# Kernel tuning notes

Measured on AMD Instinct MI355X. Metric: run time of the kernel, lower is better.

## Reference

```python
import jax, jax.numpy as jnp
import numpy as np

BN_EPS = 1e-5

def _conv1x1(x, w, b):
    # x: [B,C,H,W], w: [O,C], b: [O] -> [B,O,H,W]
    return jnp.einsum('bchw,oc->bohw', x, w) + b[None, :, None, None]

def setup_inputs() -> dict:
    key = jax.random.key(0)
    ks = jax.random.split(key, 9)
    B, C, H, W = 8, 256, 64, 64
    I = C // 2
    s_in = 1.0 / np.sqrt(C)
    s_out = 1.0 / np.sqrt(I)
    return {
        'x':       jax.random.normal(ks[0], (B, C, H, W), dtype=jnp.float32),
        'g_w':     jax.random.uniform(ks[1], (I, C), jnp.float32, -s_in, s_in),
        'g_b':     jax.random.uniform(ks[2], (I,),  jnp.float32, -s_in, s_in),
        'theta_w': jax.random.uniform(ks[3], (I, C), jnp.float32, -s_in, s_in),
        'theta_b': jax.random.uniform(ks[4], (I,),  jnp.float32, -s_in, s_in),
        'phi_w':   jax.random.uniform(ks[5], (I, C), jnp.float32, -s_in, s_in),
        'phi_b':   jax.random.uniform(ks[6], (I,),  jnp.float32, -s_in, s_in),
        'w_w':     jax.random.uniform(ks[7], (C, I), jnp.float32, -s_out, s_out),
        'w_b':     jax.random.uniform(ks[8], (C,),  jnp.float32, -s_out, s_out),
        'gamma':   jnp.ones((C,), dtype=jnp.float32),   # BN weight init constant 1
        'beta':    jnp.zeros((C,), dtype=jnp.float32),  # BN bias init constant 0
    }

def reference(x, g_w, g_b, theta_w, theta_b, phi_w, phi_b, w_w, w_b, gamma, beta):
    B, C, H, W = x.shape
    I = g_w.shape[0]
    N = H * W
    g_x     = _conv1x1(x, g_w, g_b).reshape(B, I, N)          # [B,I,N]
    theta_x = _conv1x1(x, theta_w, theta_b).reshape(B, I, N)  # [B,I,N]
    phi_x   = _conv1x1(x, phi_w, phi_b).reshape(B, I, N)      # [B,I,N]
    # f = theta^T @ phi : [B,N,N]
    f = jnp.einsum('bin,bim->bnm', theta_x, phi_x)
    a = jax.nn.softmax(f, axis=-1)
    # y = a @ g^T : [B,N,I] -> [B,I,H,W]
    y = jnp.einsum('bnm,bim->bin', a, g_x).reshape(B, I, H, W)
    wy = _conv1x1(y, w_w, w_b)                                # [B,C,H,W]
    # BatchNorm2d (training mode: batch statistics over B,H,W per channel)
    mean = jnp.mean(wy, axis=(0, 2, 3), keepdims=True)
    var = jnp.var(wy, axis=(0, 2, 3), keepdims=True)
    wy_bn = (wy - mean) * jax.lax.rsqrt(var + BN_EPS)
    wy_bn = wy_bn * gamma[None, :, None, None] + beta[None, :, None, None]
    return wy_bn + x
```

## Files before the change

### kernel.cpp

```cpp
#include <hip/hip_runtime.h>

#define B_ 8
#define C_ 256
#define I_ 128
#define N_ 4096
#define BN_ (B_ * N_)
#define LOG2E 1.4426950408889634f

typedef __attribute__((ext_vector_type(8))) short bf16x8;
typedef __attribute__((ext_vector_type(4))) float f32x4;
typedef __attribute__((ext_vector_type(2))) int i32x2;

static __device__ __forceinline__ short f2bf(float f) {
    unsigned u = __float_as_uint(f);
    unsigned r = u + 0x7fffu + ((u >> 16) & 1u);
    return (short)(r >> 16);
}
static __device__ __forceinline__ float bf2f(short s) {
    return __uint_as_float(((unsigned)(unsigned short)s) << 16);
}
static __device__ __forceinline__ unsigned cvt_pk_bf16(float lo, float hi) {
    unsigned r;
    asm("v_cvt_pk_bf16_f32 %0, %1, %2" : "=v"(r) : "v"(lo), "v"(hi));
    return r;
}

__global__ void k_prep(const float* g_w, const float* theta_w, const float* phi_w,
                       const float* g_b, const float* theta_b, const float* phi_b,
                       const float* w_w, short* wcat, short* wwb, float* bcat) {
    int i = blockIdx.x * 256 + threadIdx.x;
    if (i < 384 * 256) {
        int j = i >> 8, c = i & 255;
        float v = (j < 128) ? theta_w[j * 256 + c] * LOG2E
                : (j < 256) ? phi_w[(j - 128) * 256 + c]
                            : g_w[(j - 256) * 256 + c];
        wcat[i] = f2bf(v);
    } else if (i < 384 * 256 + 256 * 128) {
        int k = i - 384 * 256;
        wwb[k] = f2bf(w_w[k]);
    } else if (i < 384 * 256 + 256 * 128 + 384) {
        int j = i - (384 * 256 + 256 * 128);
        bcat[j] = (j < 128) ? theta_b[j] * LOG2E
                : (j < 256) ? phi_b[j - 128] : g_b[j - 256];
    }
}

__global__ __launch_bounds__(256) void k_proj(const float* __restrict__ x,
                                              const short* __restrict__ wcat,
                                              const float* __restrict__ bcat,
                                              short* __restrict__ tp,
                                              short* __restrict__ gmat) {
    int b = blockIdx.y;
    int n0 = blockIdx.x * 64;
    int tid = threadIdx.x;
    int wave = tid >> 6, lane = tid & 63, s = lane & 15, q = lane >> 4;
    __shared__ short xs[64][264];

#pragma unroll
    for (int it = 0; it < 16; ++it) {
        int cr = (tid >> 4) + it * 16;
        int nc = tid & 15;
        const float4 v = *(const float4*)&x[((size_t)b * C_ + cr) * N_ + n0 + nc * 4];
        xs[nc * 4 + 0][cr] = f2bf(v.x);
        xs[nc * 4 + 1][cr] = f2bf(v.y);
        xs[nc * 4 + 2][cr] = f2bf(v.z);
        xs[nc * 4 + 3][cr] = f2bf(v.w);
    }
    __syncthreads();

    f32x4 acc[4][6];
#pragma unroll
    for (int rt = 0; rt < 4; ++rt)
#pragma unroll
        for (int jt = 0; jt < 6; ++jt) acc[rt][jt] = (f32x4){0.f, 0.f, 0.f, 0.f};

#pragma unroll
    for (int kb = 0; kb < 8; ++kb) {
        bf16x8 af[4], bfv[6];
#pragma unroll
        for (int rt = 0; rt < 4; ++rt)
            af[rt] = *(const bf16x8*)&xs[rt * 16 + s][kb * 32 + q * 8];
#pragma unroll
        for (int jt = 0; jt < 6; ++jt)
            bfv[jt] = *(const bf16x8*)&wcat[(wave * 96 + jt * 16 + s) * 256 + kb * 32 + q * 8];
#pragma unroll
        for (int rt = 0; rt < 4; ++rt)
#pragma unroll
            for (int jt = 0; jt < 6; ++jt)
                acc[rt][jt] = __builtin_amdgcn_mfma_f32_16x16x32_bf16(af[rt], bfv[jt], acc[rt][jt], 0, 0, 0);
    }

#pragma unroll
    for (int rt = 0; rt < 4; ++rt)
#pragma unroll
        for (int jt = 0; jt < 6; ++jt) {
            int j = wave * 96 + jt * 16 + s;
            float bias = bcat[j];
#pragma unroll
            for (int r = 0; r < 4; ++r) {
                int n = n0 + rt * 16 + 4 * q + r;
                float v = acc[rt][jt][r] + bias;
                if (j < 256)
                    tp[((size_t)b * N_ + n) * 256 + j] = f2bf(v);
                else
                    gmat[((size_t)b * I_ + (j - 256)) * N_ + n] = f2bf(v);
            }
        }
}

__global__ __launch_bounds__(256) void k_attn(const short* __restrict__ tp,
                                              const short* __restrict__ gmat,
                                              float* __restrict__ Op,
                                              float* __restrict__ lbuf) {
    int id = blockIdx.x;
    int b = id & 7;
    int qt = (id >> 3) & 31;
    int half = id >> 8;
    int n0 = qt * 128;
    int tid = threadIdx.x;
    int wave = tid >> 6, lane = tid & 63, s = lane & 15, q = lane >> 4;

    __shared__ __align__(16) short Kt[64 * 128];
    __shared__ __align__(16) short Vt[128 * 64];
    __shared__ __align__(16) short Pl[4 * 32 * 64];

    char* KtB = (char*)Kt;
    char* VtB = (char*)Vt;
    char* PlB = (char*)Pl;

    const int swz = (s & 7) << 4;
    int kA[4];
#pragma unroll
    for (int kb = 0; kb < 4; ++kb) kA[kb] = s * 256 + ((kb * 64 + q * 16) ^ swz);
    int vA[2];
    int pR[2];
#pragma unroll
    for (int kb2 = 0; kb2 < 2; ++kb2) {
        int col = (kb2 * 64 + q * 16) ^ swz;
        vA[kb2] = s * 128 + col;
        pR[kb2] = wave * 4096 + s * 128 + col;
    }
    int pW[4];
#pragma unroll
    for (int tc = 0; tc < 4; ++tc)
        pW[tc] = wave * 4096 + s * 128 + ((tc * 32 + q * 8) ^ swz);
    int krow = tid >> 4, kch = tid & 15;
    int vrow = tid >> 3, vch = tid & 7;
    int kW = krow * 256 + ((kch * 16) ^ ((krow & 7) << 4));
    int vW = vrow * 128 + ((vch * 16) ^ ((vrow & 7) << 4));

    bf16x8 qf[2][4];
#pragma unroll
    for (int fr = 0; fr < 2; ++fr) {
        const short* qb = tp + ((size_t)b * N_ + n0 + wave * 32 + fr * 16 + s) * 256;
#pragma unroll
        for (int kb = 0; kb < 4; ++kb) qf[fr][kb] = *(const bf16x8*)(qb + kb * 32 + q * 8);
    }

    f32x4 ot[2][8];
#pragma unroll
    for (int fr = 0; fr < 2; ++fr)
#pragma unroll
        for (int t = 0; t < 8; ++t) ot[fr][t] = (f32x4){0.f, 0.f, 0.f, 0.f};
    float lsum[2] = {0.f, 0.f};

    const int mStart = half * 2048, mEnd = mStart + 2048;

    bf16x8 pk[4], pv[4];
#pragma unroll
    for (int it = 0; it < 4; ++it) {
        pk[it] = *(const bf16x8*)&tp[((size_t)b * N_ + mStart + krow + it * 16) * 256 + 128 + kch * 8];
        pv[it] = *(const bf16x8*)&gmat[((size_t)b * I_ + vrow + it * 32) * N_ + mStart + vch * 8];
    }

    for (int m0 = mStart; m0 < mEnd; m0 += 64) {
        __syncthreads();
#pragma unroll
        for (int it = 0; it < 4; ++it) {
            *(bf16x8*)(KtB + kW + it * 4096) = pk[it];
            *(bf16x8*)(VtB + vW + it * 4096) = pv[it];
        }
        __syncthreads();
        if (m0 + 64 < mEnd) {
#pragma unroll
            for (int it = 0; it < 4; ++it) {
                pk[it] = *(const bf16x8*)&tp[((size_t)b * N_ + m0 + 64 + krow + it * 16) * 256 + 128 + kch * 8];
                pv[it] = *(const bf16x8*)&gmat[((size_t)b * I_ + vrow + it * 32) * N_ + m0 + 64 + vch * 8];
            }
        }

        f32x4 sa[2][4];
#pragma unroll
        for (int fr = 0; fr < 2; ++fr)
#pragma unroll
            for (int tc = 0; tc < 4; ++tc) sa[fr][tc] = (f32x4){0.f, 0.f, 0.f, 0.f};
#pragma unroll
        for (int tc = 0; tc < 4; ++tc) {
            bf16x8 bfv[4];
#pragma unroll
            for (int kb = 0; kb < 4; ++kb)
                bfv[kb] = *(const bf16x8*)(KtB + kA[kb] + tc * 4096);
#pragma unroll
            for (int fr = 0; fr < 2; ++fr)
#pragma unroll
                for (int kb = 0; kb < 4; ++kb)
                    sa[fr][tc] = __builtin_amdgcn_mfma_f32_16x16x32_bf16(bfv[kb], qf[fr][kb], sa[fr][tc], 0, 0, 0);
        }

#pragma unroll
        for (int fr = 0; fr < 2; ++fr) {
#pragma unroll
            for (int tc = 0; tc < 4; ++tc)
#pragma unroll
                for (int r = 0; r < 4; ++r) sa[fr][tc][r] = exp2f(sa[fr][tc][r]);
            float t0 = (sa[fr][0][0] + sa[fr][0][1]) + (sa[fr][0][2] + sa[fr][0][3]);
            float t1 = (sa[fr][1][0] + sa[fr][1][1]) + (sa[fr][1][2] + sa[fr][1][3]);
            float t2 = (sa[fr][2][0] + sa[fr][2][1]) + (sa[fr][2][2] + sa[fr][2][3]);
            float t3 = (sa[fr][3][0] + sa[fr][3][1]) + (sa[fr][3][2] + sa[fr][3][3]);
            lsum[fr] += (t0 + t1) + (t2 + t3);
#pragma unroll
            for (int tc = 0; tc < 4; ++tc) {
                i32x2 w;
                w.x = (int)cvt_pk_bf16(sa[fr][tc][0], sa[fr][tc][1]);
                w.y = (int)cvt_pk_bf16(sa[fr][tc][2], sa[fr][tc][3]);
                *(i32x2*)(PlB + pW[tc] + fr * 2048) = w;
            }
        }

#pragma unroll
        for (int kb2 = 0; kb2 < 2; ++kb2) {
            bf16x8 pa0 = *(const bf16x8*)(PlB + pR[kb2]);
            bf16x8 pa1 = *(const bf16x8*)(PlB + pR[kb2] + 2048);
#pragma unroll
            for (int t = 0; t < 8; ++t) {
                bf16x8 vb = *(const bf16x8*)(VtB + vA[kb2] + t * 2048);
                ot[0][t] = __builtin_amdgcn_mfma_f32_16x16x32_bf16(pa0, vb, ot[0][t], 0, 0, 0);
                ot[1][t] = __builtin_amdgcn_mfma_f32_16x16x32_bf16(pa1, vb, ot[1][t], 0, 0, 0);
            }
        }
    }

#pragma unroll
    for (int fr = 0; fr < 2; ++fr) {
        lsum[fr] += __shfl_xor(lsum[fr], 16);
        lsum[fr] += __shfl_xor(lsum[fr], 32);
    }
    if (q == 0) {
#pragma unroll
        for (int fr = 0; fr < 2; ++fr) {
            size_t row = (size_t)half * BN_ + (size_t)b * N_ + n0 + wave * 32 + fr * 16 + s;
            lbuf[row] = lsum[fr];
        }
    }

#pragma unroll
    for (int fr = 0; fr < 2; ++fr) {
        size_t rbase = (size_t)half * BN_ + (size_t)b * N_ + n0 + wave * 32 + fr * 16 + 4 * q;
#pragma unroll
        for (int t = 0; t < 8; ++t)
#pragma unroll
            for (int r = 0; r < 4; ++r)
                Op[(rbase + r) * I_ + t * 16 + s] = ot[fr][t][r];
    }
}

__global__ __launch_bounds__(256) void k_wy(const float* __restrict__ Op,
                                            const float* __restrict__ lbuf,
                                            const short* __restrict__ wwb,
                                            const float* __restrict__ w_b,
                                            short* __restrict__ wyh) {
    int b = blockIdx.y;
    int n0 = blockIdx.x * 64;
    int tid = threadIdx.x;
    int wave = tid >> 6, lane = tid & 63, s = lane & 15, q = lane >> 4;

    float linv[4];
#pragma unroll
    for (int nt = 0; nt < 4; ++nt) {
        size_t rn = (size_t)b * N_ + n0 + nt * 16 + s;
        linv[nt] = 1.0f / (lbuf[rn] + lbuf[(size_t)BN_ + rn]);
    }

    f32x4 acc[4][4];
#pragma unroll
    for (int ct = 0; ct < 4; ++ct)
#pragma unroll
        for (int nt = 0; nt < 4; ++nt) acc[ct][nt] = (f32x4){0.f, 0.f, 0.f, 0.f};
#pragma unroll
    for (int kb = 0; kb < 4; ++kb) {
        bf16x8 af[4], bfv[4];
#pragma unroll
        for (int ct = 0; ct < 4; ++ct)
            af[ct] = *(const bf16x8*)&wwb[(wave * 64 + ct * 16 + s) * 128 + kb * 32 + q * 8];
#pragma unroll
        for (int nt = 0; nt < 4; ++nt) {
            size_t rn = (size_t)b * N_ + n0 + nt * 16 + s;
            const float* p1 = Op + rn * I_ + kb * 32 + q * 8;
            const float* p2 = p1 + (size_t)BN_ * I_;
            float4 a0 = *(const float4*)p1;
            float4 a1 = *(const float4*)(p1 + 4);
            float4 b0 = *(const float4*)p2;
            float4 b1 = *(const float4*)(p2 + 4);
            short v[8];
            v[0] = f2bf((a0.x + b0.x) * linv[nt]);
            v[1] = f2bf((a0.y + b0.y) * linv[nt]);
            v[2] = f2bf((a0.z + b0.z) * linv[nt]);
            v[3] = f2bf((a0.w + b0.w) * linv[nt]);
            v[4] = f2bf((a1.x + b1.x) * linv[nt]);
            v[5] = f2bf((a1.y + b1.y) * linv[nt]);
            v[6] = f2bf((a1.z + b1.z) * linv[nt]);
            v[7] = f2bf((a1.w + b1.w) * linv[nt]);
            bfv[nt] = *(const bf16x8*)v;
        }
#pragma unroll
        for (int ct = 0; ct < 4; ++ct)
#pragma unroll
            for (int nt = 0; nt < 4; ++nt)
                acc[ct][nt] = __builtin_amdgcn_mfma_f32_16x16x32_bf16(af[ct], bfv[nt], acc[ct][nt], 0, 0, 0);
    }
#pragma unroll
    for (int ct = 0; ct < 4; ++ct)
#pragma unroll
        for (int nt = 0; nt < 4; ++nt)
#pragma unroll
            for (int r = 0; r < 4; ++r) {
                int c = wave * 64 + ct * 16 + 4 * q + r;
                int n = n0 + nt * 16 + s;
                wyh[((size_t)b * C_ + c) * N_ + n] = f2bf(acc[ct][nt][r] + w_b[c]);
            }
}

__global__ __launch_bounds__(256) void k_stats(const short* __restrict__ wyh,
                                               const float* __restrict__ gamma,
                                               const float* __restrict__ beta,
                                               float* __restrict__ scale,
                                               float* __restrict__ shift) {
    int c = blockIdx.x;
    int tid = threadIdx.x;
    float s1 = 0.f, s2 = 0.f;
    for (int b = 0; b < B_; ++b) {
        const short* p = wyh + ((size_t)b * C_ + c) * N_;
        for (int idx = tid * 8; idx < N_; idx += 2048) {
            bf16x8 v = *(const bf16x8*)&p[idx];
#pragma unroll
            for (int j = 0; j < 8; ++j) {
                float f = bf2f(v[j]);
                s1 += f;
                s2 += f * f;
            }
        }
    }
#pragma unroll
    for (int off = 1; off < 64; off <<= 1) {
        s1 += __shfl_xor(s1, off);
        s2 += __shfl_xor(s2, off);
    }
    __shared__ float r1[4], r2[4];
    if ((tid & 63) == 0) { r1[tid >> 6] = s1; r2[tid >> 6] = s2; }
    __syncthreads();
    if (tid == 0) {
        float t1 = r1[0] + r1[1] + r1[2] + r1[3];
        float t2 = r2[0] + r2[1] + r2[2] + r2[3];
        const float inv = 1.0f / 32768.0f;
        float mean = t1 * inv;
        float var = t2 * inv - mean * mean;
        float sc = gamma[c] * rsqrtf(var + 1e-5f);
        scale[c] = sc;
        shift[c] = beta[c] - mean * sc;
    }
}

__global__ __launch_bounds__(256) void k_out(const short* __restrict__ wyh,
                                             const float* __restrict__ x,
                                             const float* __restrict__ scale,
                                             const float* __restrict__ shift,
                                             float* __restrict__ out) {
    int gid = blockIdx.x * 256 + threadIdx.x;
    size_t base = (size_t)gid * 8;
    int c = (int)((base >> 12) & 255);
    float sc = scale[c], sh = shift[c];
    bf16x8 w = *(const bf16x8*)&wyh[base];
    float4 x0 = *(const float4*)&x[base];
    float4 x1 = *(const float4*)&x[base + 4];
    float4 o0, o1;
    o0.x = bf2f(w[0]) * sc + sh + x0.x;
    o0.y = bf2f(w[1]) * sc + sh + x0.y;
    o0.z = bf2f(w[2]) * sc + sh + x0.z;
    o0.w = bf2f(w[3]) * sc + sh + x0.w;
    o1.x = bf2f(w[4]) * sc + sh + x1.x;
    o1.y = bf2f(w[5]) * sc + sh + x1.y;
    o1.z = bf2f(w[6]) * sc + sh + x1.z;
    o1.w = bf2f(w[7]) * sc + sh + x1.w;
    *(float4*)&out[base] = o0;
    *(float4*)&out[base + 4] = o1;
}

extern "C" void kernel_launch(void* const* d_in, const int* in_sizes, int n_in,
                              void* d_out, int out_size, void* d_ws, size_t ws_size,
                              hipStream_t stream) {
    const float* x       = (const float*)d_in[0];
    const float* g_w     = (const float*)d_in[1];
    const float* g_b     = (const float*)d_in[2];
    const float* theta_w = (const float*)d_in[3];
    const float* theta_b = (const float*)d_in[4];
    const float* phi_w   = (const float*)d_in[5];
    const float* phi_b   = (const float*)d_in[6];
    const float* w_w     = (const float*)d_in[7];
    const float* w_b     = (const float*)d_in[8];
    const float* gamma   = (const float*)d_in[9];
    const float* beta    = (const float*)d_in[10];

    char* ws = (char*)d_ws;
    size_t off = 0;
    auto alloc = [&](size_t bytes) {
        void* p = ws + off;
        off += (bytes + 255) & ~(size_t)255;
        return p;
    };
    short*  wcat  = (short*)alloc((size_t)384 * 256 * 2);
    short*  wwb   = (short*)alloc((size_t)256 * 128 * 2);
    float*  bcat  = (float*)alloc((size_t)384 * 4);
    float*  scale = (float*)alloc(256 * 4);
    float*  shift = (float*)alloc(256 * 4);
    short*  tp    = (short*)alloc((size_t)BN_ * 256 * 2);
    short*  gmat  = (short*)alloc((size_t)B_ * I_ * N_ * 2);
    short*  wyh   = (short*)alloc((size_t)BN_ * C_ * 2);
    float*  lbuf  = (float*)alloc((size_t)2 * BN_ * 4);
    float*  Op    = (float*)d_out;

    k_prep<<<514, 256, 0, stream>>>(g_w, theta_w, phi_w, g_b, theta_b, phi_b, w_w,
                                    wcat, wwb, bcat);
    k_proj<<<dim3(64, 8), 256, 0, stream>>>(x, wcat, bcat, tp, gmat);
    k_attn<<<512, 256, 0, stream>>>(tp, gmat, Op, lbuf);
    k_wy<<<dim3(64, 8), 256, 0, stream>>>(Op, lbuf, wwb, w_b, wyh);
    k_stats<<<256, 256, 0, stream>>>(wyh, gamma, beta, scale, shift);
    k_out<<<4096, 256, 0, stream>>>(wyh, x, scale, shift, (float*)d_out);
}
```

Before: 253.0 us.

## Keep P in registers via permlane swaps and double K/V tile size

The attention kernel no longer round-trips the exponentiated score tile through LDS. It rearranges the bf16-packed P fragments into the MFMA A-operand layout in registers using v_permlane32_swap and v_permlane16_swap. The key/value tile per iteration grows from 64 to 128 keys, halving the barrier count, and the K and V tiles now share one swizzled store pattern. It also adds s_setprio around MFMA blocks and launch_bounds(256,2), at the cost of more prefetch registers and LDS per block, which may cap occupancy.

```diff
diff --git a/kernel.cpp b/kernel.cpp
--- a/kernel.cpp
+++ b/kernel.cpp
@@ -9,7 +9,7 @@
 
 typedef __attribute__((ext_vector_type(8))) short bf16x8;
 typedef __attribute__((ext_vector_type(4))) float f32x4;
-typedef __attribute__((ext_vector_type(2))) int i32x2;
+typedef __attribute__((ext_vector_type(4))) int i32x4;
 
 static __device__ __forceinline__ short f2bf(float f) {
     unsigned u = __float_as_uint(f);
@@ -108,10 +108,10 @@
         }
 }
 
-__global__ __launch_bounds__(256) void k_attn(const short* __restrict__ tp,
-                                              const short* __restrict__ gmat,
-                                              float* __restrict__ Op,
-                                              float* __restrict__ lbuf) {
+__global__ __launch_bounds__(256, 2) void k_attn(const short* __restrict__ tp,
+                                                 const short* __restrict__ gmat,
+                                                 float* __restrict__ Op,
+                                                 float* __restrict__ lbuf) {
     int id = blockIdx.x;
     int b = id & 7;
     int qt = (id >> 3) & 31;
@@ -120,34 +120,22 @@
     int tid = threadIdx.x;
     int wave = tid >> 6, lane = tid & 63, s = lane & 15, q = lane >> 4;
 
-    __shared__ __align__(16) short Kt[64 * 128];
-    __shared__ __align__(16) short Vt[128 * 64];
-    __shared__ __align__(16) short Pl[4 * 32 * 64];
+    __shared__ __align__(16) short Kt[128 * 128];
+    __shared__ __align__(16) short Vt[128 * 128];
 
     char* KtB = (char*)Kt;
     char* VtB = (char*)Vt;
-    char* PlB = (char*)Pl;
 
     const int swz = (s & 7) << 4;
     int kA[4];
 #pragma unroll
     for (int kb = 0; kb < 4; ++kb) kA[kb] = s * 256 + ((kb * 64 + q * 16) ^ swz);
     int vA[2];
-    int pR[2];
-#pragma unroll
-    for (int kb2 = 0; kb2 < 2; ++kb2) {
-        int col = (kb2 * 64 + q * 16) ^ swz;
-        vA[kb2] = s * 128 + col;
-        pR[kb2] = wave * 4096 + s * 128 + col;
-    }
-    int pW[4];
-#pragma unroll
-    for (int tc = 0; tc < 4; ++tc)
-        pW[tc] = wave * 4096 + s * 128 + ((tc * 32 + q * 8) ^ swz);
+#pragma unroll
+    for (int kb2 = 0; kb2 < 2; ++kb2)
+        vA[kb2] = s * 256 + ((kb2 * 64 + q * 16) ^ swz);
     int krow = tid >> 4, kch = tid & 15;
-    int vrow = tid >> 3, vch = tid & 7;
-    int kW = krow * 256 + ((kch * 16) ^ ((krow & 7) << 4));
-    int vW = vrow * 128 + ((vch * 16) ^ ((vrow & 7) << 4));
+    int stW = krow * 256 + ((kch * 16) ^ ((krow & 7) << 4));
 
     bf16x8 qf[2][4];
 #pragma unroll
@@ -166,76 +154,97 @@
 
     const int mStart = half * 2048, mEnd = mStart + 2048;
 
-    bf16x8 pk[4], pv[4];
-#pragma unroll
-    for (int it = 0; it < 4; ++it) {
+    bf16x8 pk[8], pv[8];
+#pragma unroll
+    for (int it = 0; it < 8; ++it) {
         pk[it] = *(const bf16x8*)&tp[((size_t)b * N_ + mStart + krow + it * 16) * 256 + 128 + kch * 8];
-        pv[it] = *(const bf16x8*)&gmat[((size_t)b * I_ + vrow + it * 32) * N_ + mStart + vch * 8];
-    }
-
-    for (int m0 = mStart; m0 < mEnd; m0 += 64) {
+        pv[it] = *(const bf16x8*)&gmat[((size_t)b * I_ + krow + it * 16) * N_ + mStart + kch * 8];
+    }
+
+    for (int m0 = mStart; m0 < mEnd; m0 += 128) {
         __syncthreads();
 #pragma unroll
-        for (int it = 0; it < 4; ++it) {
-            *(bf16x8*)(KtB + kW + it * 4096) = pk[it];
-            *(bf16x8*)(VtB + vW + it * 4096) = pv[it];
+        for (int it = 0; it < 8; ++it) {
+            *(bf16x8*)(KtB + stW + it * 4096) = pk[it];
+            *(bf16x8*)(VtB + stW + it * 4096) = pv[it];
         }
         __syncthreads();
-        if (m0 + 64 < mEnd) {
-#pragma unroll
-            for (int it = 0; it < 4; ++it) {
-                pk[it] = *(const bf16x8*)&tp[((size_t)b * N_ + m0 + 64 + krow + it * 16) * 256 + 128 + kch * 8];
-                pv[it] = *(const bf16x8*)&gmat[((size_t)b * I_ + vrow + it * 32) * N_ + m0 + 64 + vch * 8];
-            }
-        }
-
-        f32x4 sa[2][4];
-#pragma unroll
-        for (int fr = 0; fr < 2; ++fr)
-#pragma unroll
-            for (int tc = 0; tc < 4; ++tc) sa[fr][tc] = (f32x4){0.f, 0.f, 0.f, 0.f};
-#pragma unroll
-        for (int tc = 0; tc < 4; ++tc) {
-            bf16x8 bfv[4];
-#pragma unroll
-            for (int kb = 0; kb < 4; ++kb)
-                bfv[kb] = *(const bf16x8*)(KtB + kA[kb] + tc * 4096);
+        if (m0 + 128 < mEnd) {
+#pragma unroll
+            for (int it = 0; it < 8; ++it) {
+                pk[it] = *(const bf16x8*)&tp[((size_t)b * N_ + m0 + 128 + krow + it * 16) * 256 + 128 + kch * 8];
+                pv[it] = *(const bf16x8*)&gmat[((size_t)b * I_ + krow + it * 16) * N_ + m0 + 128 + kch * 8];
+            }
+        }
+
+#pragma unroll
+        for (int h = 0; h < 2; ++h) {
+            const int hK = h * 16384;
+            const int hV = h * 128;
+
+            f32x4 sa[2][4];
 #pragma unroll
             for (int fr = 0; fr < 2; ++fr)
 #pragma unroll
+                for (int tc = 0; tc < 4; ++tc) sa[fr][tc] = (f32x4){0.f, 0.f, 0.f, 0.f};
+            __builtin_amdgcn_s_setprio(1);
+#pragma unroll
+            for (int tc = 0; tc < 4; ++tc) {
+                bf16x8 bfv[4];
+#pragma unroll
                 for (int kb = 0; kb < 4; ++kb)
-                    sa[fr][tc] = __builtin_amdgcn_mfma_f32_16x16x32_bf16(bfv[kb], qf[fr][kb], sa[fr][tc], 0, 0, 0);
-        }
-
-#pragma unroll
-        for (int fr = 0; fr < 2; ++fr) {
-#pragma unroll
-            for (int tc = 0; tc < 4; ++tc)
-#pragma unroll
-                for (int r = 0; r < 4; ++r) sa[fr][tc][r] = exp2f(sa[fr][tc][r]);
-            float t0 = (sa[fr][0][0] + sa[fr][0][1]) + (sa[fr][0][2] + sa[fr][0][3]);
-            float t1 = (sa[fr][1][0] + sa[fr][1][1]) + (sa[fr][1][2] + sa[fr][1][3]);
-            float t2 = (sa[fr][2][0] + sa[fr][2][1]) + (sa[fr][2][2] + sa[fr][2][3]);
-            float t3 = (sa[fr][3][0] + sa[fr][3][1]) + (sa[fr][3][2] + sa[fr][3][3]);
-            lsum[fr] += (t0 + t1) + (t2 + t3);
-#pragma unroll
-            for (int tc = 0; tc < 4; ++tc) {
-                i32x2 w;
-                w.x = (int)cvt_pk_bf16(sa[fr][tc][0], sa[fr][tc][1]);
-                w.y = (int)cvt_pk_bf16(sa[fr][tc][2], sa[fr][tc][3]);
-                *(i32x2*)(PlB + pW[tc] + fr * 2048) = w;
-            }
-        }
-
-#pragma unroll
-        for (int kb2 = 0; kb2 < 2; ++kb2) {
-            bf16x8 pa0 = *(const bf16x8*)(PlB + pR[kb2]);
-            bf16x8 pa1 = *(const bf16x8*)(PlB + pR[kb2] + 2048);
-#pragma unroll
-            for (int t = 0; t < 8; ++t) {
-                bf16x8 vb = *(const bf16x8*)(VtB + vA[kb2] + t * 2048);
-                ot[0][t] = __builtin_amdgcn_mfma_f32_16x16x32_bf16(pa0, vb, ot[0][t], 0, 0, 0);
-                ot[1][t] = __builtin_amdgcn_mfma_f32_16x16x32_bf16(pa1, vb, ot[1][t], 0, 0, 0);
+                    bfv[kb] = *(const bf16x8*)(KtB + hK + kA[kb] + tc * 4096);
+#pragma unroll
+                for (int fr = 0; fr < 2; ++fr)
+#pragma unroll
+                    for (int kb = 0; kb < 4; ++kb)
+                        sa[fr][tc] = __builtin_amdgcn_mfma_f32_16x16x32_bf16(bfv[kb], qf[fr][kb], sa[fr][tc], 0, 0, 0);
+            }
+            __builtin_amdgcn_s_setprio(0);
+
+            unsigned W[2][4][2];
+#pragma unroll
+            for (int fr = 0; fr < 2; ++fr) {
+#pragma unroll
+                for (int tc = 0; tc < 4; ++tc)
+#pragma unroll
+                    for (int r = 0; r < 4; ++r) sa[fr][tc][r] = exp2f(sa[fr][tc][r]);
+                float t0 = (sa[fr][0][0] + sa[fr][0][1]) + (sa[fr][0][2] + sa[fr][0][3]);
+                float t1 = (sa[fr][1][0] + sa[fr][1][1]) + (sa[fr][1][2] + sa[fr][1][3]);
+                float t2 = (sa[fr][2][0] + sa[fr][2][1]) + (sa[fr][2][2] + sa[fr][2][3]);
+                float t3 = (sa[fr][3][0] + sa[fr][3][1]) + (sa[fr][3][2] + sa[fr][3][3]);
+                lsum[fr] += (t0 + t1) + (t2 + t3);
+#pragma unroll
+                for (int tc = 0; tc < 4; ++tc) {
+                    W[fr][tc][0] = cvt_pk_bf16(sa[fr][tc][0], sa[fr][tc][1]);
+                    W[fr][tc][1] = cvt_pk_bf16(sa[fr][tc][2], sa[fr][tc][3]);
+                }
+            }
+
+#pragma unroll
+            for (int kb2 = 0; kb2 < 2; ++kb2) {
+                bf16x8 pa[2];
+#pragma unroll
+                for (int fr = 0; fr < 2; ++fr) {
+                    unsigned rA = W[fr][2 * kb2 + 0][0];
+                    unsigned rB = W[fr][2 * kb2 + 0][1];
+                    unsigned rC = W[fr][2 * kb2 + 1][0];
+                    unsigned rD = W[fr][2 * kb2 + 1][1];
+                    asm("v_permlane32_swap_b32 %0, %1" : "+v"(rA), "+v"(rC));
+                    asm("v_permlane32_swap_b32 %0, %1" : "+v"(rB), "+v"(rD));
+                    asm("v_permlane16_swap_b32 %0, %1" : "+v"(rA), "+v"(rC));
+                    asm("v_permlane16_swap_b32 %0, %1" : "+v"(rB), "+v"(rD));
+                    i32x4 wv = (i32x4){(int)rA, (int)rB, (int)rC, (int)rD};
+                    pa[fr] = __builtin_bit_cast(bf16x8, wv);
+                }
+                __builtin_amdgcn_s_setprio(1);
+#pragma unroll
+                for (int t = 0; t < 8; ++t) {
+                    bf16x8 vb = *(const bf16x8*)(VtB + hV + vA[kb2] + t * 4096);
+                    ot[0][t] = __builtin_amdgcn_mfma_f32_16x16x32_bf16(pa[0], vb, ot[0][t], 0, 0, 0);
+                    ot[1][t] = __builtin_amdgcn_mfma_f32_16x16x32_bf16(pa[1], vb, ot[1][t], 0, 0, 0);
+                }
+                __builtin_amdgcn_s_setprio(0);
             }
         }
     }
```

After: 265.8 us. 1.05x slower.
